# Kernel optimization log

Measured on AMD Instinct MI355X. Metric: run time of the kernel, lower is better.

The kernel has to match this reference:

```python
import jax, jax.numpy as jnp
import numpy as np

B, T, C, H = 4, 2048, 768, 12
D = C // H  # head dim = 64


def setup_inputs() -> dict:
    key = jax.random.key(0)
    ks = jax.random.split(key, 4)
    scale = 0.02
    return {
        "x": jax.random.normal(ks[0], (B, T, C), dtype=jnp.float32),
        "W_attn": jax.random.normal(ks[1], (C, 3 * C), dtype=jnp.float32) * scale,
        "b_attn": jnp.zeros((3 * C,), dtype=jnp.float32),
        "W_proj": jax.random.normal(ks[2], (C, C), dtype=jnp.float32) * scale,
        "b_proj": jnp.zeros((C,), dtype=jnp.float32),
    }


def reference(x, W_attn, b_attn, W_proj, b_proj):
    Bsz, Tlen, Cdim = x.shape
    qkv = x @ W_attn + b_attn                    # [B,T,3C]
    q, k, v = jnp.split(qkv, 3, axis=-1)          # each [B,T,C]
    # [B,T,C] -> [B,H,T,D]
    def heads(t):
        return t.reshape(Bsz, Tlen, H, D).transpose(0, 2, 1, 3)
    q, k, v = heads(q), heads(k), heads(v)
    att = jnp.einsum("bhqd,bhkd->bhqk", q, k) * (1.0 / np.sqrt(D))
    # causal mask: position q attends to k <= q
    mask = jnp.tril(jnp.ones((Tlen, Tlen), dtype=bool))
    att = jnp.where(mask[None, None], att, -jnp.inf)
    att = jax.nn.softmax(att, axis=-1)
    y = jnp.einsum("bhqk,bhkd->bhqd", att, v)     # [B,H,T,D]
    y = y.transpose(0, 2, 1, 3).reshape(Bsz, Tlen, Cdim)
    return y @ W_proj + b_proj
```

## Files before the change

### kernel.cpp

```cpp
#include <hip/hip_runtime.h>

#define B_SZ   4
#define T_LEN  2048
#define C_DIM  768
#define H_NUM  12
#define THREEC (3 * C_DIM)

typedef _Float16 f16;
typedef _Float16 half8 __attribute__((ext_vector_type(8)));
typedef _Float16 half4 __attribute__((ext_vector_type(4)));
typedef float    f32x4 __attribute__((ext_vector_type(4)));

#define GLD16(gaddr, laddr)                                                         \
  __builtin_amdgcn_global_load_lds(                                                 \
      (const __attribute__((address_space(1))) unsigned int*)(gaddr),               \
      (__attribute__((address_space(3))) unsigned int*)(laddr), 16, 0, 0)
#define MFMA16(a, b, c) __builtin_amdgcn_mfma_f32_16x16x32_f16(a, b, c, 0, 0, 0)

__global__ __launch_bounds__(256) void cast_f32_f16_kernel(
    const float* __restrict__ src, f16* __restrict__ dst, int n8) {
  int i = blockIdx.x * 256 + threadIdx.x;
  if (i >= n8) return;
  const float* s = src + (size_t)i * 8;
  half8 h;
#pragma unroll
  for (int u = 0; u < 8; ++u) h[u] = (f16)s[u];
  *(half8*)(dst + (size_t)i * 8) = h;
}

__global__ __launch_bounds__(256) void transpose_cast2_kernel(
    const float* __restrict__ Wa, const float* __restrict__ Wp,
    f16* __restrict__ WtA, f16* __restrict__ WtP) {
  __shared__ f16 tile[32][33];
  int bx = blockIdx.x;
  const float* W; f16* Wt; int N;
  if (bx < THREEC / 32) { W = Wa; Wt = WtA; N = THREEC; }
  else { W = Wp; Wt = WtP; N = C_DIM; bx -= THREEC / 32; }
  const int n0 = bx * 32, k0 = blockIdx.y * 32;
  const int tx = threadIdx.x & 31, ty = threadIdx.x >> 5;
#pragma unroll
  for (int i = 0; i < 4; ++i)
    tile[ty + i * 8][tx] = (f16)W[(size_t)(k0 + ty + i * 8) * N + n0 + tx];
  __syncthreads();
#pragma unroll
  for (int i = 0; i < 4; ++i)
    Wt[(size_t)(n0 + ty + i * 8) * C_DIM + k0 + tx] = tile[tx][ty + i * 8];
}

template <int BM, int BN, int OUT_F16>
__global__ __launch_bounds__(256) void gemm_f16_kernel(
    const f16* __restrict__ A, const f16* __restrict__ Bt,
    const float* __restrict__ bias, f16* __restrict__ OutH,
    float* __restrict__ OutF, int M, int N, int K) {
  __shared__ f16 As[BM * 32];
  __shared__ f16 Bs[BN * 32];
  const int tid = threadIdx.x;
  const int lane = tid & 63, wave = tid >> 6;
  const int lm = lane & 15, kq = lane >> 4;
  constexpr int MT = BM / 32, NT = BN / 32;
  const int wm = (wave & 1) * (BM / 2), wn = (wave >> 1) * (BN / 2);
  const int row0 = blockIdx.y * BM, col0 = blockIdx.x * BN;
  const int rp = kq ^ (lm & 3);

  f32x4 acc[MT][NT] = {};

  for (int k0 = 0; k0 < K; k0 += 32) {
    __syncthreads();
#pragma unroll
    for (int i = 0; i < BM / 64; ++i) {
      int c = tid + i * 256;
      int cc = (c & 3) ^ ((c >> 2) & 3);
      GLD16(&A[(size_t)(row0 + (c >> 2)) * K + k0 + cc * 8],
            &As[(i * 256 + wave * 64) * 8]);
    }
#pragma unroll
    for (int i = 0; i < BN / 64; ++i) {
      int c = tid + i * 256;
      int cc = (c & 3) ^ ((c >> 2) & 3);
      GLD16(&Bt[(size_t)(col0 + (c >> 2)) * K + k0 + cc * 8],
            &Bs[(i * 256 + wave * 64) * 8]);
    }
    __syncthreads();
    half8 af[MT], bf[NT];
#pragma unroll
    for (int t = 0; t < MT; ++t)
      af[t] = *(const half8*)&As[(wm + t * 16 + lm) * 32 + rp * 8];
#pragma unroll
    for (int t = 0; t < NT; ++t)
      bf[t] = *(const half8*)&Bs[(wn + t * 16 + lm) * 32 + rp * 8];
#pragma unroll
    for (int mt = 0; mt < MT; ++mt)
#pragma unroll
      for (int nt = 0; nt < NT; ++nt)
        acc[mt][nt] = MFMA16(af[mt], bf[nt], acc[mt][nt]);
  }

#pragma unroll
  for (int mt = 0; mt < MT; ++mt) {
    const int row = row0 + wm + mt * 16 + kq * 4;
#pragma unroll
    for (int nt = 0; nt < NT; ++nt) {
      const int col = col0 + wn + nt * 16 + lm;
      const float bv = bias[col];
#pragma unroll
      for (int r = 0; r < 4; ++r) {
        float v = acc[mt][nt][r] + bv;
        if (OUT_F16)
          OutH[(size_t)(row + r) * N + col] = (f16)v;
        else
          OutF[(size_t)(row + r) * N + col] = v;
      }
    }
  }
}

__global__ __launch_bounds__(256) void v_transpose_kernel(
    const f16* __restrict__ qkv, f16* __restrict__ vt) {
  __shared__ f16 tile[64 * 68];
  const int bh = blockIdx.x, b = bh / H_NUM, h = bh % H_NUM;
  const int t0 = blockIdx.y * 64;
  const int tid = threadIdx.x;
#pragma unroll
  for (int i = 0; i < 2; ++i) {
    int c = tid + i * 256;
    int tr = c >> 3, doff = (c & 7) * 8;
    half8 v = *(const half8*)&qkv[(size_t)(b * T_LEN + t0 + tr) * THREEC + 2 * C_DIM + h * 64 + doff];
#pragma unroll
    for (int u = 0; u < 8; ++u) tile[(doff + u) * 68 + tr] = v[u];
  }
  __syncthreads();
#pragma unroll
  for (int i = 0; i < 2; ++i) {
    int c = tid + i * 256;
    int d = c >> 3, toff = (c & 7) * 8;
    half8 v;
#pragma unroll
    for (int u = 0; u < 8; ++u) v[u] = tile[d * 68 + toff + u];
    *(half8*)&vt[((size_t)bh * 64 + d) * T_LEN + t0 + toff] = v;
  }
}

__global__ __launch_bounds__(256) void attn_kernel(
    const f16* __restrict__ qkv, const f16* __restrict__ vt,
    f16* __restrict__ y) {
  __shared__ f16 Kt[64 * 64];
  __shared__ f16 Vt[64 * 64];
  __shared__ f16 Pl[4][32 * 64];

  const int bh = blockIdx.x, b = bh / H_NUM, h = bh % H_NUM;
  const int q0 = (15 - (int)blockIdx.y) * 128;
  const int tid = threadIdx.x, lane = tid & 63, wave = tid >> 6;
  const int lm = lane & 15, kq = lane >> 4, lm7 = lm & 7;
  const int qw = q0 + wave * 32;
  const f16 qscale = (f16)(0.125f * 1.44269504f);

  half8 bq[2][2];
#pragma unroll
  for (int qt = 0; qt < 2; ++qt)
#pragma unroll
    for (int c2 = 0; c2 < 2; ++c2) {
      half8 v = *(const half8*)&qkv[(size_t)(b * T_LEN + qw + qt * 16 + lm) * THREEC +
                                    h * 64 + c2 * 32 + kq * 8];
      bq[qt][c2] = v * qscale;
    }

  f32x4 o[2][4] = {};
  float lsum[2] = {0.f, 0.f};

  const int r0 = tid >> 3, c0 = ((tid & 7) ^ (r0 & 7)) * 8;
  const int s1 = tid + 256, r1 = s1 >> 3, c1 = ((s1 & 7) ^ (r1 & 7)) * 8;
  const f16* kp0 = &qkv[(size_t)(b * T_LEN + r0) * THREEC + C_DIM + h * 64 + c0];
  const f16* kp1 = &qkv[(size_t)(b * T_LEN + r1) * THREEC + C_DIM + h * 64 + c1];
  const f16* vp0 = &vt[((size_t)bh * 64 + r0) * T_LEN + c0];
  const f16* vp1 = &vt[((size_t)bh * 64 + r1) * T_LEN + c1];

  const int n_tiles = q0 / 64 + 2;
  for (int it = 0; it < n_tiles; ++it) {
    const int j0 = it * 64;
    __syncthreads();
    GLD16(kp0, &Kt[(wave * 64) * 8]);        kp0 += (size_t)64 * THREEC;
    GLD16(kp1, &Kt[(256 + wave * 64) * 8]);  kp1 += (size_t)64 * THREEC;
    GLD16(vp0, &Vt[(wave * 64) * 8]);        vp0 += 64;
    GLD16(vp1, &Vt[(256 + wave * 64) * 8]);  vp1 += 64;
    __syncthreads();

    if (j0 <= qw + 31) {
      f32x4 s4[2][4];
#pragma unroll
      for (int ct = 0; ct < 4; ++ct) {
        const f16* kr = &Kt[(ct * 16 + lm) * 64];
        half8 ak0 = *(const half8*)&kr[(kq ^ lm7) * 8];
        half8 ak1 = *(const half8*)&kr[((4 + kq) ^ lm7) * 8];
#pragma unroll
        for (int qt = 0; qt < 2; ++qt) {
          f32x4 z = {};
          z = MFMA16(ak0, bq[qt][0], z);
          s4[qt][ct] = MFMA16(ak1, bq[qt][1], z);
        }
      }
      if (j0 + 63 > qw) {
#pragma unroll
        for (int qt = 0; qt < 2; ++qt) {
          const int qrow = qw + qt * 16 + lm;
#pragma unroll
          for (int ct = 0; ct < 4; ++ct)
#pragma unroll
            for (int r = 0; r < 4; ++r)
              if (j0 + ct * 16 + kq * 4 + r > qrow) s4[qt][ct][r] = -1e30f;
        }
      }
#pragma unroll
      for (int qt = 0; qt < 2; ++qt) {
        f16* prow = &Pl[wave][(qt * 16 + lm) * 64];
#pragma unroll
        for (int ct = 0; ct < 4; ++ct) {
          half4 pk;
#pragma unroll
          for (int r = 0; r < 4; ++r) {
            float e = exp2f(s4[qt][ct][r]);
            lsum[qt] += e;
            pk[r] = (f16)e;
          }
          *(half4*)&prow[(((ct * 2 + (kq >> 1)) ^ lm7) * 8) + (kq & 1) * 4] = pk;
        }
      }
      __asm__ volatile("s_waitcnt lgkmcnt(0)" ::: "memory");
      half8 bv0[4], bv1[4];
#pragma unroll
      for (int dt = 0; dt < 4; ++dt) {
        const f16* vr = &Vt[(dt * 16 + lm) * 64];
        bv0[dt] = *(const half8*)&vr[(kq ^ lm7) * 8];
        bv1[dt] = *(const half8*)&vr[((4 + kq) ^ lm7) * 8];
      }
#pragma unroll
      for (int qt = 0; qt < 2; ++qt) {
        const f16* pr = &Pl[wave][(qt * 16 + lm) * 64];
        half8 ap0 = *(const half8*)&pr[(kq ^ lm7) * 8];
        half8 ap1 = *(const half8*)&pr[((4 + kq) ^ lm7) * 8];
#pragma unroll
        for (int dt = 0; dt < 4; ++dt) {
          o[qt][dt] = MFMA16(ap0, bv0[dt], o[qt][dt]);
          o[qt][dt] = MFMA16(ap1, bv1[dt], o[qt][dt]);
        }
      }
    }
  }

#pragma unroll
  for (int qt = 0; qt < 2; ++qt) {
    lsum[qt] += __shfl_xor(lsum[qt], 16, 64);
    lsum[qt] += __shfl_xor(lsum[qt], 32, 64);
#pragma unroll
    for (int r = 0; r < 4; ++r) {
      const float lr = __shfl(lsum[qt], kq * 4 + r, 64);
      const float inv = 1.f / lr;
      const size_t base =
          (size_t)(b * T_LEN + qw + qt * 16 + kq * 4 + r) * C_DIM + h * 64;
#pragma unroll
      for (int dt = 0; dt < 4; ++dt)
        y[base + dt * 16 + lm] = (f16)(o[qt][dt][r] * inv);
    }
  }
}

extern "C" void kernel_launch(void* const* d_in, const int* in_sizes, int n_in,
                              void* d_out, int out_size, void* d_ws, size_t ws_size,
                              hipStream_t stream) {
  const float* x      = (const float*)d_in[0];
  const float* W_attn = (const float*)d_in[1];
  const float* b_attn = (const float*)d_in[2];
  const float* W_proj = (const float*)d_in[3];
  const float* b_proj = (const float*)d_in[4];
  float* out = (float*)d_out;

  const int M = B_SZ * T_LEN;
  auto align256 = [](size_t v) { return (v + 255) & ~(size_t)255; };
  char* ws = (char*)d_ws;
  f16* xh   = (f16*)ws; ws += align256((size_t)M * C_DIM * 2);
  f16* WtA  = (f16*)ws; ws += align256((size_t)THREEC * C_DIM * 2);
  f16* WtP  = (f16*)ws; ws += align256((size_t)C_DIM * C_DIM * 2);
  f16* qkvh = (f16*)ws; ws += align256((size_t)M * THREEC * 2);
  f16* vtg  = (f16*)ws; ws += align256((size_t)B_SZ * H_NUM * 64 * T_LEN * 2);
  f16* yh   = (f16*)ws; ws += align256((size_t)M * C_DIM * 2);

  {
    int n8 = M * C_DIM / 8;
    cast_f32_f16_kernel<<<(n8 + 255) / 256, 256, 0, stream>>>(x, xh, n8);
  }
  transpose_cast2_kernel<<<dim3((THREEC + C_DIM) / 32, C_DIM / 32), 256, 0, stream>>>(
      W_attn, W_proj, WtA, WtP);

  gemm_f16_kernel<128, 128, 1><<<dim3(THREEC / 128, M / 128), 256, 0, stream>>>(
      xh, WtA, b_attn, qkvh, nullptr, M, THREEC, C_DIM);

  v_transpose_kernel<<<dim3(B_SZ * H_NUM, T_LEN / 64), 256, 0, stream>>>(qkvh, vtg);

  attn_kernel<<<dim3(B_SZ * H_NUM, 16), 256, 0, stream>>>(qkvh, vtg, yh);

  gemm_f16_kernel<128, 64, 0><<<dim3(C_DIM / 64, M / 128), 256, 0, stream>>>(
      yh, WtP, b_proj, nullptr, out, M, C_DIM, C_DIM);
}
```

Before: 226.0 us.

## Pair causal query chunks per block with 2-wave blocks and MFMA row sums

```diff
diff --git a/kernel.cpp b/kernel.cpp
--- a/kernel.cpp
+++ b/kernel.cpp
@@ -140,51 +140,69 @@
   }
 }
 
-__global__ __launch_bounds__(256) void attn_kernel(
+__global__ __launch_bounds__(128) void attn_kernel(
     const f16* __restrict__ qkv, const f16* __restrict__ vt,
     f16* __restrict__ y) {
   __shared__ f16 Kt[64 * 64];
   __shared__ f16 Vt[64 * 64];
-  __shared__ f16 Pl[4][32 * 64];
+  __shared__ f16 Pl[2][32 * 64];
 
   const int bh = blockIdx.x, b = bh / H_NUM, h = bh % H_NUM;
-  const int q0 = (15 - (int)blockIdx.y) * 128;
   const int tid = threadIdx.x, lane = tid & 63, wave = tid >> 6;
   const int lm = lane & 15, kq = lane >> 4, lm7 = lm & 7;
-  const int qw = q0 + wave * 32;
   const f16 qscale = (f16)(0.125f * 1.44269504f);
 
-  half8 bq[2][2];
-#pragma unroll
-  for (int qt = 0; qt < 2; ++qt)
-#pragma unroll
-    for (int c2 = 0; c2 < 2; ++c2) {
-      half8 v = *(const half8*)&qkv[(size_t)(b * T_LEN + qw + qt * 16 + lm) * THREEC +
-                                    h * 64 + c2 * 32 + kq * 8];
-      bq[qt][c2] = v * qscale;
-    }
-
-  f32x4 o[2][4] = {};
-  float lsum[2] = {0.f, 0.f};
-
-  const int r0 = tid >> 3, c0 = ((tid & 7) ^ (r0 & 7)) * 8;
-  const int s1 = tid + 256, r1 = s1 >> 3, c1 = ((s1 & 7) ^ (r1 & 7)) * 8;
-  const f16* kp0 = &qkv[(size_t)(b * T_LEN + r0) * THREEC + C_DIM + h * 64 + c0];
-  const f16* kp1 = &qkv[(size_t)(b * T_LEN + r1) * THREEC + C_DIM + h * 64 + c1];
-  const f16* vp0 = &vt[((size_t)bh * 64 + r0) * T_LEN + c0];
-  const f16* vp1 = &vt[((size_t)bh * 64 + r1) * T_LEN + c1];
-
-  const int n_tiles = q0 / 64 + 2;
-  for (int it = 0; it < n_tiles; ++it) {
-    const int j0 = it * 64;
-    __syncthreads();
-    GLD16(kp0, &Kt[(wave * 64) * 8]);        kp0 += (size_t)64 * THREEC;
-    GLD16(kp1, &Kt[(256 + wave * 64) * 8]);  kp1 += (size_t)64 * THREEC;
-    GLD16(vp0, &Vt[(wave * 64) * 8]);        vp0 += 64;
-    GLD16(vp1, &Vt[(256 + wave * 64) * 8]);  vp1 += 64;
-    __syncthreads();
-
-    if (j0 <= qw + 31) {
+  half8 vones;
+#pragma unroll
+  for (int u = 0; u < 8; ++u) vones[u] = (f16)1.f;
+
+  int srow[4], scol[4];
+#pragma unroll
+  for (int i = 0; i < 4; ++i) {
+    int s = tid + i * 128;
+    srow[i] = s >> 3;
+    scol[i] = ((s & 7) ^ (srow[i] & 7)) * 8;
+  }
+
+  for (int half = 0; half < 2; ++half) {
+    const int c = (half == 0) ? (31 - (int)blockIdx.y) : (int)blockIdx.y;
+    const int q0 = c * 64;
+    const int qw = q0 + wave * 32;
+
+    half8 bq[2][2];
+#pragma unroll
+    for (int qt = 0; qt < 2; ++qt)
+#pragma unroll
+      for (int c2 = 0; c2 < 2; ++c2) {
+        half8 v = *(const half8*)&qkv[(size_t)(b * T_LEN + qw + qt * 16 + lm) * THREEC +
+                                      h * 64 + c2 * 32 + kq * 8];
+        bq[qt][c2] = v * qscale;
+      }
+
+    f32x4 o[2][4] = {};
+    f32x4 ol[2] = {};
+
+    const f16* kp[4];
+    const f16* vp[4];
+#pragma unroll
+    for (int i = 0; i < 4; ++i) {
+      kp[i] = &qkv[(size_t)(b * T_LEN + srow[i]) * THREEC + C_DIM + h * 64 + scol[i]];
+      vp[i] = &vt[((size_t)bh * 64 + srow[i]) * T_LEN + scol[i]];
+    }
+
+    const int n_tiles = q0 / 64 + 1;
+    for (int it = 0; it < n_tiles; ++it) {
+      const int j0 = it * 64;
+      __syncthreads();
+#pragma unroll
+      for (int i = 0; i < 4; ++i) {
+        GLD16(kp[i], &Kt[(i * 128 + wave * 64) * 8]);
+        kp[i] += (size_t)64 * THREEC;
+        GLD16(vp[i], &Vt[(i * 128 + wave * 64) * 8]);
+        vp[i] += 64;
+      }
+      __syncthreads();
+
       f32x4 s4[2][4];
 #pragma unroll
       for (int ct = 0; ct < 4; ++ct) {
@@ -216,11 +234,7 @@
         for (int ct = 0; ct < 4; ++ct) {
           half4 pk;
 #pragma unroll
-          for (int r = 0; r < 4; ++r) {
-            float e = exp2f(s4[qt][ct][r]);
-            lsum[qt] += e;
-            pk[r] = (f16)e;
-          }
+          for (int r = 0; r < 4; ++r) pk[r] = (f16)exp2f(s4[qt][ct][r]);
           *(half4*)&prow[(((ct * 2 + (kq >> 1)) ^ lm7) * 8) + (kq & 1) * 4] = pk;
         }
       }
@@ -242,24 +256,24 @@
           o[qt][dt] = MFMA16(ap0, bv0[dt], o[qt][dt]);
           o[qt][dt] = MFMA16(ap1, bv1[dt], o[qt][dt]);
         }
-      }
-    }
-  }
-
-#pragma unroll
-  for (int qt = 0; qt < 2; ++qt) {
-    lsum[qt] += __shfl_xor(lsum[qt], 16, 64);
-    lsum[qt] += __shfl_xor(lsum[qt], 32, 64);
-#pragma unroll
-    for (int r = 0; r < 4; ++r) {
-      const float lr = __shfl(lsum[qt], kq * 4 + r, 64);
-      const float inv = 1.f / lr;
-      const size_t base =
-          (size_t)(b * T_LEN + qw + qt * 16 + kq * 4 + r) * C_DIM + h * 64;
-#pragma unroll
-      for (int dt = 0; dt < 4; ++dt)
-        y[base + dt * 16 + lm] = (f16)(o[qt][dt][r] * inv);
-    }
+        ol[qt] = MFMA16(ap0, vones, ol[qt]);
+        ol[qt] = MFMA16(ap1, vones, ol[qt]);
+      }
+    }
+
+#pragma unroll
+    for (int qt = 0; qt < 2; ++qt) {
+#pragma unroll
+      for (int r = 0; r < 4; ++r) {
+        const float inv = 1.f / ol[qt][r];
+        const size_t base =
+            (size_t)(b * T_LEN + qw + qt * 16 + kq * 4 + r) * C_DIM + h * 64;
+#pragma unroll
+        for (int dt = 0; dt < 4; ++dt)
+          y[base + dt * 16 + lm] = (f16)(o[qt][dt][r] * inv);
+      }
+    }
+    __syncthreads();
   }
 }
 
@@ -295,7 +309,7 @@
 
   v_transpose_kernel<<<dim3(B_SZ * H_NUM, T_LEN / 64), 256, 0, stream>>>(qkvh, vtg);
 
-  attn_kernel<<<dim3(B_SZ * H_NUM, 16), 256, 0, stream>>>(qkvh, vtg, yh);
+  attn_kernel<<<dim3(B_SZ * H_NUM, 16), 128, 0, stream>>>(qkvh, vtg, yh);
 
   gemm_f16_kernel<128, 64, 0><<<dim3(C_DIM / 64, M / 128), 256, 0, stream>>>(
       yh, WtP, b_proj, nullptr, out, M, C_DIM, C_DIM);
```

Measured after the change: 237.7 us. 1.05x slower.
